# Performance work log

Hardware: AMD Instinct MI355X
Metric: run time of the kernel (lower is better)

The kernel has to match this reference:

```python
import jax, jax.numpy as jnp
import numpy as np

BS, H, W = 2, 24, 24
WIDTH = 20
M1 = M2 = 12
N = H * W
NPAIR = N * (N - 1) // 2
COLL_COEF = 0.9  # training=True path (eval path zeroes the collision term entirely)
_IU, _JU = np.triu_indices(N, k=1)  # static pair indices


def _gelu(x):
    return jax.nn.gelu(x, approximate=False)  # torch F.gelu default = exact erf


def _spectral(x, wr, wi):
    # x: (bs, c, h, w); wr/wi: (2, c, c, M1, M2) -> weights1, weights2
    bs, c, h, w = x.shape
    xft = jnp.fft.rfft2(x)  # (bs, c, h, w//2+1) complex64
    w1 = wr[0] + 1j * wi[0]
    w2 = wr[1] + 1j * wi[1]
    top = jnp.einsum('bixy,ioxy->boxy', xft[:, :, :M1, :M2], w1)
    bot = jnp.einsum('bixy,ioxy->boxy', xft[:, :, -M1:, :M2], w2)
    out = jnp.zeros((bs, c, h, w // 2 + 1), dtype=xft.dtype)
    out = out.at[:, :, :M1, :M2].set(top).at[:, :, -M1:, :M2].set(bot)
    return jnp.fft.irfft2(out, s=(h, w))


def _pair_norm(d):
    # d: (bs, c, n, n) -> (bs, n, n); eps keeps grad finite on the zero diagonal
    return jnp.sqrt(jnp.sum(d * d, axis=1) + 1e-12)


def _kinet_dsmc(p, a, vec):
    # p plays the role of x-positions; v = a*dt (dt=1) exactly as in the torch code
    bs, c, h, w = p.shape
    n = h * w
    x = p.reshape(bs, c, n)
    v = a.reshape(bs, c, n)  # v = a * dt
    x_r = _pair_norm(x[:, :, :, None] - x[:, :, None, :])       # (bs, n, n)
    v_r = _pair_norm(v[:, :, :, None] - v[:, :, None, :])       # (bs, n, n)
    v_cm = (v[:, :, :, None] + v[:, :, None, :]) * 0.5          # (bs, c, n, n)
    u_x = jnp.exp(-x_r)
    v_r_max = jnp.max(v_r, axis=(1, 2), keepdims=True)          # (bs, 1, 1)
    mask = v_r / v_r_max * u_x
    cmask = (mask > 1.0 - COLL_COEF).astype(p.dtype)            # (bs, n, n)
    # antisymmetric projection: R[:, :, i, j] = vec_pair for i<j, -vec_pair for i>j, 0 diag
    R = jnp.zeros((bs, c, n, n), p.dtype)
    R = R.at[:, :, _IU, _JU].set(vec).at[:, :, _JU, _IU].set(-vec)
    v_r_leaving = v_r[:, None] * R                               # (bs, c, n, n)
    delta_v = v_cm + v_r_leaving - v[:, :, :, None]
    v_new = v + jnp.sum(delta_v * cmask[:, None], axis=2)
    x_new = x + v_new  # dt = 1
    return x_new.reshape(bs, c, h, w), v_new.reshape(bs, c, h, w)


def _rv_step(rv, ori, s):
    rv = rv * ori + ori + s
    return rv / jnp.linalg.norm(rv, axis=1, keepdims=True)


def _forward(x, v, fc0_w, fc0_b, sc_wr, sc_wi, w_k, w_b, fc1_w, fc1_b, fc2_w, fc2_b, rv_init, rv_s):
    bs, h, w, _ = x.shape
    gx = jnp.broadcast_to(jnp.linspace(0.0, 1.0, h, dtype=x.dtype)[None, :, None, None], (bs, h, w, 1))
    gy = jnp.broadcast_to(jnp.linspace(0.0, 1.0, w, dtype=x.dtype)[None, None, :, None], (bs, h, w, 1))
    x = jnp.concatenate([x, gx, gy], axis=-1)          # (bs, h, w, 12)
    x = x @ fc0_w + fc0_b                              # lift to width
    x = jnp.transpose(x, (0, 3, 1, 2))                 # (bs, width, h, w)
    ori = rv_init / jnp.linalg.norm(rv_init, axis=1, keepdims=True)
    rv = rv_init
    for k in range(4):
        a = _spectral(x, sc_wr[k], sc_wi[k])
        p = jnp.einsum('bchw,oc->bohw', x, w_k[k]) + w_b[k][None, :, None, None]
        rv = _rv_step(rv, ori, rv_s[k])
        x, v = _kinet_dsmc(p, a, rv)
        if k < 3:
            x = _gelu(x)
            v = _gelu(v)
    x = jnp.transpose(x, (0, 2, 3, 1))                 # (bs, h, w, width)
    x = _gelu(x @ fc1_w + fc1_b)
    x = x @ fc2_w + fc2_b
    return x


def setup_inputs() -> dict:
    key = jax.random.key(0)
    ks = jax.random.split(key, 12)
    f = jnp.float32
    scale = 1.0 / (WIDTH * WIDTH)
    xs = -4.0 - 3.0 * jax.random.uniform(ks[9], (4,), f)                 # in [-7, -4]
    signs = jax.random.randint(ks[10], (4,), 0, 2).astype(f) * 2.0 - 1.0
    return {
        'x': jax.random.normal(ks[0], (BS, H, W, 10), f),
        'v': jax.random.normal(ks[1], (BS, WIDTH, H, W), f),
        'fc0_w': jax.random.normal(ks[2], (12, WIDTH), f) * 0.1,
        'fc0_b': jnp.zeros((WIDTH,), f),
        'sc_wr': jax.random.uniform(ks[3], (4, 2, WIDTH, WIDTH, M1, M2), f) * scale,
        'sc_wi': jax.random.uniform(ks[4], (4, 2, WIDTH, WIDTH, M1, M2), f) * scale,
        'w_k': jax.random.normal(ks[5], (4, WIDTH, WIDTH), f) * 0.1,
        'w_b': jnp.zeros((4, WIDTH), f),
        'fc1_w': jax.random.normal(ks[6], (WIDTH, 128), f) * 0.1,
        'fc1_b': jnp.zeros((128,), f),
        'fc2_w': jax.random.normal(ks[7], (128, 1), f) * 0.1,
        'fc2_b': jnp.zeros((1,), f),
        'rv_init': jax.random.normal(ks[8], (BS, WIDTH, NPAIR), f),
        'rv_s': signs * jnp.exp(xs),
    }


def reference(x, v, fc0_w, fc0_b, sc_wr, sc_wi, w_k, w_b, fc1_w, fc1_b, fc2_w, fc2_b, rv_init, rv_s):
    return _forward(x, v, fc0_w, fc0_b, sc_wr, sc_wi, w_k, w_b, fc1_w, fc1_b, fc2_w, fc2_b, rv_init, rv_s)
```

## Files before the change

kernel.cpp:

```cpp
#include <hip/hip_runtime.h>


#define N_     576
#define NPAIR_ 165600
#define C_     20

__device__ __forceinline__ float gelu_f(float x){
    return 0.5f * x * (1.0f + erff(x * 0.70710678118654752440f));
}

__global__ void k_lift(const float* __restrict__ xin, const float* __restrict__ w,
                       const float* __restrict__ b, float* __restrict__ xo){
    int t = blockIdx.x*blockDim.x + threadIdx.x;
    if (t >= 2*N_) return;
    int hw = t % N_;
    int h = hw / 24, wc = hw % 24;
    float in[12];
    const float* xp = xin + (size_t)t*10;
    #pragma unroll
    for (int q=0;q<10;q++) in[q] = xp[q];
    in[10] = (float)h  * (1.0f/23.0f);
    in[11] = (float)wc * (1.0f/23.0f);
    #pragma unroll
    for (int c=0;c<C_;c++){
        float acc = b[c];
        #pragma unroll
        for (int q=0;q<12;q++) acc += in[q]*w[q*C_+c];
        xo[(size_t)(t/N_)*C_*N_ + (size_t)c*N_ + hw] = acc;
    }
}

__global__ void k_tr(const float* __restrict__ rvi, float* __restrict__ rvt){
    int t = blockIdx.x*blockDim.x + threadIdx.x;
    if (t >= 2*NPAIR_) return;
    int bb = t / NPAIR_; int pr = t % NPAIR_;
    size_t ibase = (size_t)bb*C_*NPAIR_ + pr;
    float v[C_];
    #pragma unroll
    for (int c=0;c<C_;c++) v[c] = rvi[ibase + (size_t)c*NPAIR_];
    float4* dst = (float4*)(rvt + (size_t)t*C_);
    #pragma unroll
    for (int q=0;q<5;q++) dst[q] = make_float4(v[4*q],v[4*q+1],v[4*q+2],v[4*q+3]);
}

__global__ void k_fft_fwd(const float* __restrict__ x, float* __restrict__ Xr, float* __restrict__ Xi){
    __shared__ float xt[576], Tr[288], Ti[288], cst[24], snt[24];
    int bc = blockIdx.x;
    int tid = threadIdx.x;
    if (tid < 24){
        float s, c;
        sincosf((float)tid * 0.26179938779914943654f, &s, &c);
        cst[tid]=c; snt[tid]=s;
    }
    for (int q=tid;q<576;q+=288) xt[q] = x[(size_t)bc*576+q];
    __syncthreads();
    {
        int h = tid/12, ky = tid%12;
        float ar=0.f, ai=0.f;
        for (int w=0;w<24;w++){
            int m = (ky*w) % 24;
            float v = xt[h*24+w];
            ar += v*cst[m];
            ai -= v*snt[m];
        }
        Tr[tid]=ar; Ti[tid]=ai;
    }
    __syncthreads();
    {
        int kx = tid/12, ky = tid%12;
        float ar=0.f, ai=0.f;
        for (int h=0;h<24;h++){
            int m = (kx*h)%24;
            float tr=Tr[h*12+ky], ti=Ti[h*12+ky];
            float cc=cst[m], ss=snt[m];
            ar += tr*cc + ti*ss;
            ai += ti*cc - tr*ss;
        }
        Xr[(size_t)bc*288 + tid] = ar;
        Xi[(size_t)bc*288 + tid] = ai;
    }
}

__global__ void k_fft_inv(const float* __restrict__ Xr, const float* __restrict__ Xi,
                          const float* __restrict__ wr, const float* __restrict__ wi,
                          float* __restrict__ a_t){
    __shared__ float Fr[288], Fi[288], Yr[288], Yi[288], cst[24], snt[24];
    int bo = blockIdx.x; int bb = bo/20, o = bo%20;
    int tid = threadIdx.x;
    if (tid < 24){
        float s, c;
        sincosf((float)tid * 0.26179938779914943654f, &s, &c);
        cst[tid]=c; snt[tid]=s;
    }
    if (tid < 288){
        int ky = tid%12, kx = tid/12;
        int half = (kx>=12) ? 1 : 0; int mx = kx - half*12;
        float ar=0.f, ai=0.f;
        for (int i=0;i<20;i++){
            float xr = Xr[(size_t)(bb*20+i)*288 + tid];
            float xi = Xi[(size_t)(bb*20+i)*288 + tid];
            size_t widx = ((((size_t)half*20+i)*20+o)*12+mx)*12+ky;
            float wrv = wr[widx], wiv = wi[widx];
            ar += xr*wrv - xi*wiv;
            ai += xr*wiv + xi*wrv;
        }
        Fr[tid]=ar; Fi[tid]=ai;
    }
    __syncthreads();
    if (tid < 288){
        int h = tid/12;
        float ar=0.f, ai=0.f;
        for (int kx=0;kx<24;kx++){
            int m=(kx*h)%24;
            float fr=Fr[kx*12 + (tid%12)], fi=Fi[kx*12 + (tid%12)];
            ar += fr*cst[m] - fi*snt[m];
            ai += fr*snt[m] + fi*cst[m];
        }
        Yr[tid]=ar*(1.0f/24.0f); Yi[tid]=ai*(1.0f/24.0f);
    }
    __syncthreads();
    {
        int h = tid/24, w = tid%24;
        float acc = Yr[h*12+0];
        #pragma unroll
        for (int ky=1;ky<12;ky++){
            int m=(ky*w)%24;
            acc += 2.0f*(Yr[h*12+ky]*cst[m] - Yi[h*12+ky]*snt[m]);
        }
        a_t[((size_t)bb*N_ + tid)*C_ + o] = acc*(1.0f/24.0f);
    }
}

__global__ void __launch_bounds__(64, 1)
k_p(const float* __restrict__ x, const float* __restrict__ wk,
    const float* __restrict__ wb, float* __restrict__ p_t){
    __shared__ float swk[400], swb[C_];
    int tid = threadIdx.x;
    for (int q=tid;q<400;q+=64) swk[q]=wk[q];
    if (tid < C_) swb[tid]=wb[tid];
    __syncthreads();
    int t = blockIdx.x*64 + tid;
    if (t >= 2*N_) return;
    int bb = t / N_, hw = t % N_;
    float xi[C_];
    #pragma unroll
    for (int c=0;c<C_;c++) xi[c] = x[(size_t)(bb*C_+c)*N_+hw];
    float accv[C_];
    #pragma unroll
    for (int o=0;o<C_;o++){
        float acc = swb[o];
        #pragma unroll
        for (int c=0;c<C_;c++) acc += xi[c]*swk[o*C_+c];
        accv[o]=acc;
    }
    float4* dst = (float4*)(p_t + (size_t)t*C_);
    #pragma unroll
    for (int q=0;q<5;q++) dst[q] = make_float4(accv[4*q],accv[4*q+1],accv[4*q+2],accv[4*q+3]);
}

__global__ void k_pair(const float* __restrict__ p_t, const float* __restrict__ a_t,
                       float* __restrict__ vr, float* __restrict__ ux, float* __restrict__ vmax){
    __shared__ float pi[C_], ai[C_], wred[9];
    int bb = blockIdx.x/N_, i = blockIdx.x%N_;
    int j = threadIdx.x;
    if (j < C_){ pi[j]=p_t[((size_t)bb*N_+i)*C_+j]; ai[j]=a_t[((size_t)bb*N_+i)*C_+j]; }
    __syncthreads();
    const float4* pj4 = (const float4*)(p_t + ((size_t)bb*N_+j)*C_);
    const float4* aj4 = (const float4*)(a_t + ((size_t)bb*N_+j)*C_);
    float ssx=0.f, ssv=0.f;
    #pragma unroll
    for (int q=0;q<5;q++){
        float4 pv = pj4[q], av = aj4[q];
        float dx, dv;
        dx = pi[4*q+0]-pv.x; dv = ai[4*q+0]-av.x; ssx += dx*dx; ssv += dv*dv;
        dx = pi[4*q+1]-pv.y; dv = ai[4*q+1]-av.y; ssx += dx*dx; ssv += dv*dv;
        dx = pi[4*q+2]-pv.z; dv = ai[4*q+2]-av.z; ssx += dx*dx; ssv += dv*dv;
        dx = pi[4*q+3]-pv.w; dv = ai[4*q+3]-av.w; ssx += dx*dx; ssv += dv*dv;
    }
    float xr  = sqrtf(ssx+1e-12f);
    float vrv = sqrtf(ssv+1e-12f);
    size_t idx = (size_t)(bb*N_+i)*N_ + j;
    ux[idx] = expf(-xr);
    vr[idx] = vrv;
    float m = vrv;
    #pragma unroll
    for (int off=32; off; off>>=1) m = fmaxf(m, __shfl_down(m, off, 64));
    if ((j&63)==0) wred[j>>6] = m;
    __syncthreads();
    if (j==0){
        float mm = wred[0];
        #pragma unroll
        for (int q=1;q<9;q++) mm = fmaxf(mm, wred[q]);
        atomicMax((unsigned int*)&vmax[bb], __float_as_uint(mm));
    }
}

__global__ void __launch_bounds__(256, 1)
k_vnew(const float* __restrict__ p_t, const float* __restrict__ a_t,
       const float* __restrict__ vr, const float* __restrict__ ux,
       const float* __restrict__ rvt, const float* __restrict__ vmax,
       const float* __restrict__ rs, int klayer,
       float* __restrict__ xout, int do_gelu){
    __shared__ short hlist[N_];
    __shared__ unsigned long long wmask[4][3];
    __shared__ int cnts[4];
    __shared__ float wacc[4][C_];
    int bb = blockIdx.x/N_, i = blockIdx.x%N_;
    int tid = threadIdx.x;
    int wid = tid>>6, lane = tid&63;
    float vm = vmax[bb];
    const float thr = 0.1f;
    const float* vrow = vr + (size_t)(bb*N_+i)*N_;
    const float* urow = ux + (size_t)(bb*N_+i)*N_;

    int jb = wid*144;
    unsigned long long m0, m1, m2;
    {
        int j = jb + lane;
        bool hit = ((vrow[j]/vm)*urow[j] > thr) && (j != i);
        m0 = __ballot(hit);
        j += 64;
        hit = ((vrow[j]/vm)*urow[j] > thr) && (j != i);
        m1 = __ballot(hit);
        j += 64;
        bool act = lane < 16;
        float vv = act ? vrow[j] : 0.f;
        float uu = act ? urow[j] : 0.f;
        hit = act && ((vv/vm)*uu > thr) && (j != i);
        m2 = __ballot(hit);
    }
    if (lane == 0){
        wmask[wid][0]=m0; wmask[wid][1]=m1; wmask[wid][2]=m2;
        cnts[wid] = (int)(__popcll(m0)+__popcll(m1)+__popcll(m2));
    }
    __syncthreads();
    int off = 0;
    #pragma unroll
    for (int w=0;w<4;w++) if (w < wid) off += cnts[w];
    int nhit = cnts[0]+cnts[1]+cnts[2]+cnts[3];
    {
        unsigned long long below = (1ULL<<lane)-1ULL;
        int base = off;
        if (m0 & (1ULL<<lane)) hlist[base + __popcll(m0 & below)] = (short)(jb + lane);
        base += (int)__popcll(m0);
        if (m1 & (1ULL<<lane)) hlist[base + __popcll(m1 & below)] = (short)(jb + 64 + lane);
        base += (int)__popcll(m1);
        if (m2 & (1ULL<<lane)) hlist[base + __popcll(m2 & below)] = (short)(jb + 128 + lane);
    }
    __syncthreads();

    float s_arr[4] = { rs[0], rs[1], rs[2], rs[3] };
    float macc[C_];
    #pragma unroll
    for (int c=0;c<C_;c++) macc[c]=0.f;

    for (int t=tid; t<nhit; t+=256){
        int j = hlist[t];
        float vrij = vrow[j];
        float sgn = (j<i) ? 1.0f : -1.0f;
        int lo = (j<i)?j:i, hi = (j<i)?i:j;
        int pidx = lo*(2*N_-lo-1)/2 + (hi-lo-1);
        float vrs = sgn*vrij;
        float st[C_];
        {
            const float4* rp = (const float4*)(rvt + ((size_t)bb*NPAIR_ + pidx)*C_);
            #pragma unroll
            for (int q=0;q<5;q++){
                float4 rr = rp[q];
                st[4*q+0]=rr.x; st[4*q+1]=rr.y; st[4*q+2]=rr.z; st[4*q+3]=rr.w;
            }
        }
        float ssq = 0.f;
        #pragma unroll
        for (int c=0;c<C_;c++) ssq += st[c]*st[c];
        float ini = 1.0f/sqrtf(ssq);
        float orc[C_];
        #pragma unroll
        for (int c=0;c<C_;c++) orc[c] = st[c]*ini;
        for (int l=0; l<=klayer; l++){
            float s = s_arr[l];
            float nq = 0.f;
            #pragma unroll
            for (int c=0;c<C_;c++){
                float nv = st[c]*orc[c] + orc[c] + s;
                st[c] = nv; nq += nv*nv;
            }
            float inn = 1.0f/sqrtf(nq);
            #pragma unroll
            for (int c=0;c<C_;c++) st[c] *= inn;
        }
        const float4* ap = (const float4*)(a_t + ((size_t)bb*N_ + j)*C_);
        #pragma unroll
        for (int q=0;q<5;q++){
            float4 aa = ap[q];
            macc[4*q+0] += vrs*st[4*q+0] - 0.5f*aa.x;
            macc[4*q+1] += vrs*st[4*q+1] - 0.5f*aa.y;
            macc[4*q+2] += vrs*st[4*q+2] - 0.5f*aa.z;
            macc[4*q+3] += vrs*st[4*q+3] - 0.5f*aa.w;
        }
    }
    #pragma unroll
    for (int off2=32; off2; off2>>=1){
        #pragma unroll
        for (int c=0;c<C_;c++) macc[c] += __shfl_xor(macc[c], off2, 64);
    }
    if (lane == 0){
        #pragma unroll
        for (int c=0;c<C_;c++) wacc[wid][c] = macc[c];
    }
    __syncthreads();
    if (tid < C_){
        int c = tid;
        float msum = wacc[0][c]+wacc[1][c]+wacc[2][c]+wacc[3][c];
        float cnt = (float)nhit;
        float vi = a_t[((size_t)bb*N_+i)*C_+c];
        float vnew = vi + 0.5f*cnt*vi + msum;
        float xn = p_t[((size_t)bb*N_+i)*C_+c] + vnew;
        if (do_gelu) xn = gelu_f(xn);
        xout[(size_t)(bb*C_+c)*N_+i] = xn;
    }
}

__global__ void k_head(const float* __restrict__ x, const float* __restrict__ w1,
                       const float* __restrict__ b1, const float* __restrict__ w2,
                       const float* __restrict__ b2, float* __restrict__ out){
    __shared__ float xi[C_];
    __shared__ float part[2];
    int pos = blockIdx.x; int bb = pos/N_, hw = pos%N_;
    int t = threadIdx.x;
    if (t < C_) xi[t] = x[(size_t)(bb*C_+t)*N_+hw];
    __syncthreads();
    float h = b1[t];
    #pragma unroll
    for (int c=0;c<C_;c++) h += xi[c]*w1[c*128+t];
    float g = gelu_f(h) * w2[t];
    #pragma unroll
    for (int off=32; off; off>>=1) g += __shfl_down(g, off, 64);
    if ((t&63)==0) part[t>>6] = g;
    __syncthreads();
    if (t==0) out[pos] = part[0] + part[1] + b2[0];
}

extern "C" void kernel_launch(void* const* d_in, const int* in_sizes, int n_in,
                              void* d_out, int out_size, void* d_ws, size_t ws_size,
                              hipStream_t stream) {
    const float* in_x   = (const float*)d_in[0];
    const float* fc0_w  = (const float*)d_in[2];
    const float* fc0_b  = (const float*)d_in[3];
    const float* sc_wr  = (const float*)d_in[4];
    const float* sc_wi  = (const float*)d_in[5];
    const float* w_k    = (const float*)d_in[6];
    const float* w_b    = (const float*)d_in[7];
    const float* fc1_w  = (const float*)d_in[8];
    const float* fc1_b  = (const float*)d_in[9];
    const float* fc2_w  = (const float*)d_in[10];
    const float* fc2_b  = (const float*)d_in[11];
    const float* rv_init= (const float*)d_in[12];
    const float* rv_s   = (const float*)d_in[13];
    float* out = (float*)d_out;
    float* ws  = (float*)d_ws;

    float* x_cur = ws;
    float* p_t   = ws + 23040;
    float* a_t   = ws + 46080;
    float* Xr    = ws + 69120;
    float* Xi    = ws + 80640;
    float* vr    = ws + 92160;
    float* ux    = ws + 755712;
    float* rvt   = ws + 1419264;
    float* vmax  = ws + 8043264;

    hipMemsetAsync(vmax, 0, 8*sizeof(float), stream);

    k_lift<<<dim3((2*N_+63)/64), 64, 0, stream>>>(in_x, fc0_w, fc0_b, x_cur);
    k_tr<<<(2*NPAIR_+255)/256, 256, 0, stream>>>(rv_init, rvt);

    for (int k=0;k<4;k++){
        const size_t woff = (size_t)k*2*20*20*144;
        k_fft_fwd<<<40, 288, 0, stream>>>(x_cur, Xr, Xi);
        k_fft_inv<<<40, 576, 0, stream>>>(Xr, Xi, sc_wr+woff, sc_wi+woff, a_t);
        k_p<<<(2*N_+63)/64, 64, 0, stream>>>(x_cur, w_k + k*400, w_b + k*20, p_t);
        k_pair<<<2*N_, N_, 0, stream>>>(p_t, a_t, vr, ux, vmax + 2*k);
        k_vnew<<<2*N_, 256, 0, stream>>>(p_t, a_t, vr, ux, rvt, vmax + 2*k, rv_s, k, x_cur, (k<3) ? 1 : 0);
    }

    k_head<<<2*N_, 128, 0, stream>>>(x_cur, fc1_w, fc1_b, fc2_w, fc2_b, out);
}
```

Measured before the change: 236.9 us.

## Recompute pairwise distances in vnew instead of materializing vr/ux matrices

The pairwise kernel no longer writes the full N×N velocity-distance and exp(-position-distance) matrices. It now only computes the per-batch max relative velocity, and the collision kernel recomputes both distances from p_t and a_t on the fly. The transpose and lift kernels are merged into one launch, and the forward FFT and the pointwise linear kernel share another, which cuts launches per layer. This trades about 2.6 MB of global writes and reads per layer for redundant distance arithmetic inside k_vnew.

```diff
diff --git a/kernel.cpp b/kernel.cpp
--- a/kernel.cpp
+++ b/kernel.cpp
@@ -4,80 +4,110 @@
 #define N_     576
 #define NPAIR_ 165600
 #define C_     20
+#define NB_TR  1294
 
 __device__ __forceinline__ float gelu_f(float x){
     return 0.5f * x * (1.0f + erff(x * 0.70710678118654752440f));
 }
 
-__global__ void k_lift(const float* __restrict__ xin, const float* __restrict__ w,
-                       const float* __restrict__ b, float* __restrict__ xo){
-    int t = blockIdx.x*blockDim.x + threadIdx.x;
-    if (t >= 2*N_) return;
-    int hw = t % N_;
-    int h = hw / 24, wc = hw % 24;
-    float in[12];
-    const float* xp = xin + (size_t)t*10;
-    #pragma unroll
-    for (int q=0;q<10;q++) in[q] = xp[q];
-    in[10] = (float)h  * (1.0f/23.0f);
-    in[11] = (float)wc * (1.0f/23.0f);
-    #pragma unroll
-    for (int c=0;c<C_;c++){
-        float acc = b[c];
-        #pragma unroll
-        for (int q=0;q<12;q++) acc += in[q]*w[q*C_+c];
-        xo[(size_t)(t/N_)*C_*N_ + (size_t)c*N_ + hw] = acc;
-    }
-}
-
-__global__ void k_tr(const float* __restrict__ rvi, float* __restrict__ rvt){
-    int t = blockIdx.x*blockDim.x + threadIdx.x;
-    if (t >= 2*NPAIR_) return;
-    int bb = t / NPAIR_; int pr = t % NPAIR_;
-    size_t ibase = (size_t)bb*C_*NPAIR_ + pr;
-    float v[C_];
-    #pragma unroll
-    for (int c=0;c<C_;c++) v[c] = rvi[ibase + (size_t)c*NPAIR_];
-    float4* dst = (float4*)(rvt + (size_t)t*C_);
-    #pragma unroll
-    for (int q=0;q<5;q++) dst[q] = make_float4(v[4*q],v[4*q+1],v[4*q+2],v[4*q+3]);
-}
-
-__global__ void k_fft_fwd(const float* __restrict__ x, float* __restrict__ Xr, float* __restrict__ Xi){
-    __shared__ float xt[576], Tr[288], Ti[288], cst[24], snt[24];
-    int bc = blockIdx.x;
-    int tid = threadIdx.x;
-    if (tid < 24){
-        float s, c;
-        sincosf((float)tid * 0.26179938779914943654f, &s, &c);
-        cst[tid]=c; snt[tid]=s;
-    }
-    for (int q=tid;q<576;q+=288) xt[q] = x[(size_t)bc*576+q];
-    __syncthreads();
-    {
-        int h = tid/12, ky = tid%12;
-        float ar=0.f, ai=0.f;
-        for (int w=0;w<24;w++){
-            int m = (ky*w) % 24;
-            float v = xt[h*24+w];
-            ar += v*cst[m];
-            ai -= v*snt[m];
-        }
-        Tr[tid]=ar; Ti[tid]=ai;
-    }
-    __syncthreads();
-    {
-        int kx = tid/12, ky = tid%12;
-        float ar=0.f, ai=0.f;
-        for (int h=0;h<24;h++){
-            int m = (kx*h)%24;
-            float tr=Tr[h*12+ky], ti=Ti[h*12+ky];
-            float cc=cst[m], ss=snt[m];
-            ar += tr*cc + ti*ss;
-            ai += ti*cc - tr*ss;
-        }
-        Xr[(size_t)bc*288 + tid] = ar;
-        Xi[(size_t)bc*288 + tid] = ai;
+__global__ void k_pre(const float* __restrict__ rvi, float* __restrict__ rvt,
+                      const float* __restrict__ xin, const float* __restrict__ w,
+                      const float* __restrict__ b, float* __restrict__ xo){
+    int bid = blockIdx.x;
+    if (bid < NB_TR){
+        int t = bid*256 + threadIdx.x;
+        if (t >= 2*NPAIR_) return;
+        int bb = t / NPAIR_; int pr = t % NPAIR_;
+        size_t ibase = (size_t)bb*C_*NPAIR_ + pr;
+        float v[C_];
+        #pragma unroll
+        for (int c=0;c<C_;c++) v[c] = rvi[ibase + (size_t)c*NPAIR_];
+        float4* dst = (float4*)(rvt + (size_t)t*C_);
+        #pragma unroll
+        for (int q=0;q<5;q++) dst[q] = make_float4(v[4*q],v[4*q+1],v[4*q+2],v[4*q+3]);
+    } else {
+        int t = (bid-NB_TR)*256 + threadIdx.x;
+        if (t >= 2*N_) return;
+        int hw = t % N_;
+        int h = hw / 24, wc = hw % 24;
+        float in[12];
+        const float* xp = xin + (size_t)t*10;
+        #pragma unroll
+        for (int q=0;q<10;q++) in[q] = xp[q];
+        in[10] = (float)h  * (1.0f/23.0f);
+        in[11] = (float)wc * (1.0f/23.0f);
+        #pragma unroll
+        for (int c=0;c<C_;c++){
+            float acc = b[c];
+            #pragma unroll
+            for (int q=0;q<12;q++) acc += in[q]*w[q*C_+c];
+            xo[(size_t)(t/N_)*C_*N_ + (size_t)c*N_ + hw] = acc;
+        }
+    }
+}
+
+__global__ void k_specp(const float* __restrict__ x, float* __restrict__ Xr, float* __restrict__ Xi,
+                        const float* __restrict__ wk, const float* __restrict__ wb,
+                        float* __restrict__ p_t){
+    if (blockIdx.x < 40){
+        __shared__ float xt[576], Tr[288], Ti[288], cst[24], snt[24];
+        int bc = blockIdx.x;
+        int tid = threadIdx.x;
+        if (tid < 24){
+            float s, c;
+            sincosf((float)tid * 0.26179938779914943654f, &s, &c);
+            cst[tid]=c; snt[tid]=s;
+        }
+        for (int q=tid;q<576;q+=288) xt[q] = x[(size_t)bc*576+q];
+        __syncthreads();
+        {
+            int h = tid/12, ky = tid%12;
+            float ar=0.f, ai=0.f;
+            for (int w=0;w<24;w++){
+                int m = (ky*w) % 24;
+                float v = xt[h*24+w];
+                ar += v*cst[m];
+                ai -= v*snt[m];
+            }
+            Tr[tid]=ar; Ti[tid]=ai;
+        }
+        __syncthreads();
+        {
+            int kx = tid/12, ky = tid%12;
+            float ar=0.f, ai=0.f;
+            for (int h=0;h<24;h++){
+                int m = (kx*h)%24;
+                float tr=Tr[h*12+ky], ti=Ti[h*12+ky];
+                float cc=cst[m], ss=snt[m];
+                ar += tr*cc + ti*ss;
+                ai += ti*cc - tr*ss;
+            }
+            Xr[(size_t)bc*288 + tid] = ar;
+            Xi[(size_t)bc*288 + tid] = ai;
+        }
+    } else {
+        __shared__ float swk[400], swb[C_];
+        int tid = threadIdx.x;
+        for (int q=tid;q<400;q+=288) swk[q]=wk[q];
+        if (tid < C_) swb[tid]=wb[tid];
+        __syncthreads();
+        int t = (blockIdx.x-40)*288 + tid;
+        if (t >= 2*N_) return;
+        int bb = t / N_, hw = t % N_;
+        float xi[C_];
+        #pragma unroll
+        for (int c=0;c<C_;c++) xi[c] = x[(size_t)(bb*C_+c)*N_+hw];
+        float accv[C_];
+        #pragma unroll
+        for (int o=0;o<C_;o++){
+            float acc = swb[o];
+            #pragma unroll
+            for (int c=0;c<C_;c++) acc += xi[c]*swk[o*C_+c];
+            accv[o]=acc;
+        }
+        float4* dst = (float4*)(p_t + (size_t)t*C_);
+        #pragma unroll
+        for (int q=0;q<5;q++) dst[q] = make_float4(accv[4*q],accv[4*q+1],accv[4*q+2],accv[4*q+3]);
     }
 }
 
@@ -131,58 +161,24 @@
     }
 }
 
-__global__ void __launch_bounds__(64, 1)
-k_p(const float* __restrict__ x, const float* __restrict__ wk,
-    const float* __restrict__ wb, float* __restrict__ p_t){
-    __shared__ float swk[400], swb[C_];
-    int tid = threadIdx.x;
-    for (int q=tid;q<400;q+=64) swk[q]=wk[q];
-    if (tid < C_) swb[tid]=wb[tid];
-    __syncthreads();
-    int t = blockIdx.x*64 + tid;
-    if (t >= 2*N_) return;
-    int bb = t / N_, hw = t % N_;
-    float xi[C_];
-    #pragma unroll
-    for (int c=0;c<C_;c++) xi[c] = x[(size_t)(bb*C_+c)*N_+hw];
-    float accv[C_];
-    #pragma unroll
-    for (int o=0;o<C_;o++){
-        float acc = swb[o];
-        #pragma unroll
-        for (int c=0;c<C_;c++) acc += xi[c]*swk[o*C_+c];
-        accv[o]=acc;
-    }
-    float4* dst = (float4*)(p_t + (size_t)t*C_);
-    #pragma unroll
-    for (int q=0;q<5;q++) dst[q] = make_float4(accv[4*q],accv[4*q+1],accv[4*q+2],accv[4*q+3]);
-}
-
-__global__ void k_pair(const float* __restrict__ p_t, const float* __restrict__ a_t,
-                       float* __restrict__ vr, float* __restrict__ ux, float* __restrict__ vmax){
-    __shared__ float pi[C_], ai[C_], wred[9];
+__global__ void k_pairmax(const float* __restrict__ a_t, float* __restrict__ vmax){
+    __shared__ float ai[C_], wred[9];
     int bb = blockIdx.x/N_, i = blockIdx.x%N_;
     int j = threadIdx.x;
-    if (j < C_){ pi[j]=p_t[((size_t)bb*N_+i)*C_+j]; ai[j]=a_t[((size_t)bb*N_+i)*C_+j]; }
-    __syncthreads();
-    const float4* pj4 = (const float4*)(p_t + ((size_t)bb*N_+j)*C_);
+    if (j < C_) ai[j]=a_t[((size_t)bb*N_+i)*C_+j];
+    __syncthreads();
     const float4* aj4 = (const float4*)(a_t + ((size_t)bb*N_+j)*C_);
-    float ssx=0.f, ssv=0.f;
+    float ssv=0.f;
     #pragma unroll
     for (int q=0;q<5;q++){
-        float4 pv = pj4[q], av = aj4[q];
-        float dx, dv;
-        dx = pi[4*q+0]-pv.x; dv = ai[4*q+0]-av.x; ssx += dx*dx; ssv += dv*dv;
-        dx = pi[4*q+1]-pv.y; dv = ai[4*q+1]-av.y; ssx += dx*dx; ssv += dv*dv;
-        dx = pi[4*q+2]-pv.z; dv = ai[4*q+2]-av.z; ssx += dx*dx; ssv += dv*dv;
-        dx = pi[4*q+3]-pv.w; dv = ai[4*q+3]-av.w; ssx += dx*dx; ssv += dv*dv;
-    }
-    float xr  = sqrtf(ssx+1e-12f);
-    float vrv = sqrtf(ssv+1e-12f);
-    size_t idx = (size_t)(bb*N_+i)*N_ + j;
-    ux[idx] = expf(-xr);
-    vr[idx] = vrv;
-    float m = vrv;
+        float4 av = aj4[q];
+        float dv;
+        dv = ai[4*q+0]-av.x; ssv += dv*dv;
+        dv = ai[4*q+1]-av.y; ssv += dv*dv;
+        dv = ai[4*q+2]-av.z; ssv += dv*dv;
+        dv = ai[4*q+3]-av.w; ssv += dv*dv;
+    }
+    float m = sqrtf(ssv+1e-12f);
     #pragma unroll
     for (int off=32; off; off>>=1) m = fmaxf(m, __shfl_down(m, off, 64));
     if ((j&63)==0) wred[j>>6] = m;
@@ -197,42 +193,50 @@
 
 __global__ void __launch_bounds__(256, 1)
 k_vnew(const float* __restrict__ p_t, const float* __restrict__ a_t,
-       const float* __restrict__ vr, const float* __restrict__ ux,
        const float* __restrict__ rvt, const float* __restrict__ vmax,
        const float* __restrict__ rs, int klayer,
        float* __restrict__ xout, int do_gelu){
+    __shared__ float pi[C_], ai[C_];
     __shared__ short hlist[N_];
-    __shared__ unsigned long long wmask[4][3];
     __shared__ int cnts[4];
     __shared__ float wacc[4][C_];
     int bb = blockIdx.x/N_, i = blockIdx.x%N_;
     int tid = threadIdx.x;
     int wid = tid>>6, lane = tid&63;
+    if (tid < C_){ pi[tid]=p_t[((size_t)bb*N_+i)*C_+tid]; ai[tid]=a_t[((size_t)bb*N_+i)*C_+tid]; }
+    __syncthreads();
     float vm = vmax[bb];
     const float thr = 0.1f;
-    const float* vrow = vr + (size_t)(bb*N_+i)*N_;
-    const float* urow = ux + (size_t)(bb*N_+i)*N_;
+    const float4* pbase = (const float4*)(p_t + (size_t)bb*N_*C_);
+    const float4* abase = (const float4*)(a_t + (size_t)bb*N_*C_);
 
     int jb = wid*144;
     unsigned long long m0, m1, m2;
     {
+        auto test = [&](int j)->bool{
+            const float4* pj = pbase + j*5;
+            const float4* aj = abase + j*5;
+            float ssx=0.f, ssv=0.f;
+            #pragma unroll
+            for (int q=0;q<5;q++){
+                float4 pv = pj[q], av = aj[q];
+                float dx, dv;
+                dx = pi[4*q+0]-pv.x; dv = ai[4*q+0]-av.x; ssx += dx*dx; ssv += dv*dv;
+                dx = pi[4*q+1]-pv.y; dv = ai[4*q+1]-av.y; ssx += dx*dx; ssv += dv*dv;
+                dx = pi[4*q+2]-pv.z; dv = ai[4*q+2]-av.z; ssx += dx*dx; ssv += dv*dv;
+                dx = pi[4*q+3]-pv.w; dv = ai[4*q+3]-av.w; ssx += dx*dx; ssv += dv*dv;
+            }
+            float vrv = sqrtf(ssv+1e-12f);
+            float uxv = expf(-sqrtf(ssx+1e-12f));
+            return ((vrv/vm)*uxv > thr) && (j != i);
+        };
         int j = jb + lane;
-        bool hit = ((vrow[j]/vm)*urow[j] > thr) && (j != i);
-        m0 = __ballot(hit);
-        j += 64;
-        hit = ((vrow[j]/vm)*urow[j] > thr) && (j != i);
-        m1 = __ballot(hit);
-        j += 64;
-        bool act = lane < 16;
-        float vv = act ? vrow[j] : 0.f;
-        float uu = act ? urow[j] : 0.f;
-        hit = act && ((vv/vm)*uu > thr) && (j != i);
-        m2 = __ballot(hit);
-    }
-    if (lane == 0){
-        wmask[wid][0]=m0; wmask[wid][1]=m1; wmask[wid][2]=m2;
-        cnts[wid] = (int)(__popcll(m0)+__popcll(m1)+__popcll(m2));
-    }
+        m0 = __ballot(test(j));
+        m1 = __ballot(test(j+64));
+        bool h2 = (lane<16) ? test(jb+128+lane) : false;
+        m2 = __ballot(h2);
+    }
+    if (lane == 0) cnts[wid] = (int)(__popcll(m0)+__popcll(m1)+__popcll(m2));
     __syncthreads();
     int off = 0;
     #pragma unroll
@@ -256,7 +260,19 @@
 
     for (int t=tid; t<nhit; t+=256){
         int j = hlist[t];
-        float vrij = vrow[j];
+        float av[C_];
+        {
+            const float4* aj = abase + j*5;
+            #pragma unroll
+            for (int q=0;q<5;q++){
+                float4 aa = aj[q];
+                av[4*q+0]=aa.x; av[4*q+1]=aa.y; av[4*q+2]=aa.z; av[4*q+3]=aa.w;
+            }
+        }
+        float ssv=0.f;
+        #pragma unroll
+        for (int c=0;c<C_;c++){ float dv = ai[c]-av[c]; ssv += dv*dv; }
+        float vrij = sqrtf(ssv+1e-12f);
         float sgn = (j<i) ? 1.0f : -1.0f;
         int lo = (j<i)?j:i, hi = (j<i)?i:j;
         int pidx = lo*(2*N_-lo-1)/2 + (hi-lo-1);
@@ -289,15 +305,8 @@
             #pragma unroll
             for (int c=0;c<C_;c++) st[c] *= inn;
         }
-        const float4* ap = (const float4*)(a_t + ((size_t)bb*N_ + j)*C_);
-        #pragma unroll
-        for (int q=0;q<5;q++){
-            float4 aa = ap[q];
-            macc[4*q+0] += vrs*st[4*q+0] - 0.5f*aa.x;
-            macc[4*q+1] += vrs*st[4*q+1] - 0.5f*aa.y;
-            macc[4*q+2] += vrs*st[4*q+2] - 0.5f*aa.z;
-            macc[4*q+3] += vrs*st[4*q+3] - 0.5f*aa.w;
-        }
+        #pragma unroll
+        for (int c=0;c<C_;c++) macc[c] += vrs*st[c] - 0.5f*av[c];
     }
     #pragma unroll
     for (int off2=32; off2; off2>>=1){
@@ -313,9 +322,9 @@
         int c = tid;
         float msum = wacc[0][c]+wacc[1][c]+wacc[2][c]+wacc[3][c];
         float cnt = (float)nhit;
-        float vi = a_t[((size_t)bb*N_+i)*C_+c];
+        float vi = ai[c];
         float vnew = vi + 0.5f*cnt*vi + msum;
-        float xn = p_t[((size_t)bb*N_+i)*C_+c] + vnew;
+        float xn = pi[c] + vnew;
         if (do_gelu) xn = gelu_f(xn);
         xout[(size_t)(bb*C_+c)*N_+i] = xn;
     }
@@ -365,23 +374,19 @@
     float* a_t   = ws + 46080;
     float* Xr    = ws + 69120;
     float* Xi    = ws + 80640;
-    float* vr    = ws + 92160;
-    float* ux    = ws + 755712;
-    float* rvt   = ws + 1419264;
-    float* vmax  = ws + 8043264;
+    float* rvt   = ws + 92160;
+    float* vmax  = ws + 6716160;
 
     hipMemsetAsync(vmax, 0, 8*sizeof(float), stream);
 
-    k_lift<<<dim3((2*N_+63)/64), 64, 0, stream>>>(in_x, fc0_w, fc0_b, x_cur);
-    k_tr<<<(2*NPAIR_+255)/256, 256, 0, stream>>>(rv_init, rvt);
+    k_pre<<<NB_TR+5, 256, 0, stream>>>(rv_init, rvt, in_x, fc0_w, fc0_b, x_cur);
 
     for (int k=0;k<4;k++){
         const size_t woff = (size_t)k*2*20*20*144;
-        k_fft_fwd<<<40, 288, 0, stream>>>(x_cur, Xr, Xi);
+        k_specp<<<44, 288, 0, stream>>>(x_cur, Xr, Xi, w_k + k*400, w_b + k*20, p_t);
         k_fft_inv<<<40, 576, 0, stream>>>(Xr, Xi, sc_wr+woff, sc_wi+woff, a_t);
-        k_p<<<(2*N_+63)/64, 64, 0, stream>>>(x_cur, w_k + k*400, w_b + k*20, p_t);
-        k_pair<<<2*N_, N_, 0, stream>>>(p_t, a_t, vr, ux, vmax + 2*k);
-        k_vnew<<<2*N_, 256, 0, stream>>>(p_t, a_t, vr, ux, rvt, vmax + 2*k, rv_s, k, x_cur, (k<3) ? 1 : 0);
+        k_pairmax<<<2*N_, N_, 0, stream>>>(a_t, vmax + 2*k);
+        k_vnew<<<2*N_, 256, 0, stream>>>(p_t, a_t, rvt, vmax + 2*k, rv_s, k, x_cur, (k<3) ? 1 : 0);
     }
 
     k_head<<<2*N_, 128, 0, stream>>>(x_cur, fc1_w, fc1_b, fc2_w, fc2_b, out);
```

After: 228.8 us. 1.04x faster.
